# Kernel tuning notes

Hardware: AMD Instinct MI355X
Metric: run time of the kernel (lower is better)

## Reference

```python
import jax, jax.numpy as jnp
import numpy as np

Q_MAX = 127.0  # int8 symmetric quant range


def setup_inputs() -> dict:
    key = jax.random.key(0)
    kx, kw, ks = jax.random.split(key, 3)
    M, K, N = 16384, 4096, 4096
    x = jax.random.normal(kx, (M, K), dtype=jnp.float32)
    # int8 weight values in [-127, 127]
    weight = jax.random.randint(kw, (N, K), -127, 128, dtype=jnp.int32).astype(jnp.int8)
    # per-output-row dequant scale, small positive values as a real quantizer would produce
    weight_scale = jax.random.uniform(ks, (N, 1), dtype=jnp.float32, minval=1e-3, maxval=1e-2)
    return {"x": x, "weight": weight, "weight_scale": weight_scale}


def reference(x, weight, weight_scale):
    # --- per-token dynamic activation quantization (get_hip_quant(per_Token)) ---
    amax = jnp.max(jnp.abs(x), axis=-1, keepdims=True)            # [M,1]
    x_scale = amax / Q_MAX                                        # [M,1]
    x_q = jnp.clip(jnp.round(x / jnp.maximum(x_scale, 1e-8)), -Q_MAX, Q_MAX)  # int8 values, kept fp32
    # --- gemm_a8w8: int8xint8 GEMM with fused dequant (row scale_a * col scale_b) ---
    acc = jnp.einsum('mk,nk->mn', x_q, weight.astype(jnp.float32),
                     preferred_element_type=jnp.float32)          # [M,N] int accumulation in fp32
    y = acc * x_scale * weight_scale.T                            # fused dequant scales
    return y  # fp32 stand-in for otype=bf16 output
```

## Files before the change

kernel.cpp:

```cpp
#include <hip/hip_runtime.h>
#include <stdint.h>

#define M_DIM 16384
#define N_DIM 4096
#define K_DIM 4096

#define BM 256
#define BN 128
#define BK 128

typedef int i32x4 __attribute__((ext_vector_type(4)));

__device__ __forceinline__ void async16(const uint8_t* g, uint8_t* l) {
    __builtin_amdgcn_global_load_lds(
        (const __attribute__((address_space(1))) void*)g,
        (__attribute__((address_space(3))) void*)l,
        16, 0, 0);
}

__global__ __launch_bounds__(256) void pack_w_kernel(const int* __restrict__ w32,
                                                     uint32_t* __restrict__ w8,
                                                     int n4) {
    int i = blockIdx.x * 256 + threadIdx.x;
    if (i < n4) {
        const int4 v = reinterpret_cast<const int4*>(w32)[i];
        uint32_t p = (uint32_t)(v.x & 255) | ((uint32_t)(v.y & 255) << 8) |
                     ((uint32_t)(v.z & 255) << 16) | ((uint32_t)(v.w & 255) << 24);
        w8[i] = p;
    }
}

__global__ __launch_bounds__(256) void quant_kernel(const float* __restrict__ x,
                                                    uint32_t* __restrict__ xq,
                                                    float* __restrict__ xscale) {
    const int m = blockIdx.x;
    const int t = threadIdx.x;
    const float4* row = reinterpret_cast<const float4*>(x + (size_t)m * K_DIM);
    float4 v[4];
    float amax = 0.0f;
#pragma unroll
    for (int i = 0; i < 4; ++i) {
        v[i] = row[t + i * 256];
        amax = fmaxf(amax, fmaxf(fmaxf(fabsf(v[i].x), fabsf(v[i].y)),
                                 fmaxf(fabsf(v[i].z), fabsf(v[i].w))));
    }
#pragma unroll
    for (int off = 32; off > 0; off >>= 1) amax = fmaxf(amax, __shfl_xor(amax, off));
    __shared__ float smax[4];
    if ((t & 63) == 0) smax[t >> 6] = amax;
    __syncthreads();
    amax = fmaxf(fmaxf(smax[0], smax[1]), fmaxf(smax[2], smax[3]));
    const float scale = amax / 127.0f;
    const float s = fmaxf(scale, 1e-8f);
    if (t == 0) xscale[m] = scale;
    uint32_t* orow = xq + (size_t)m * (K_DIM / 4);
#pragma unroll
    for (int i = 0; i < 4; ++i) {
        int q0 = __float2int_rn(v[i].x / s);
        int q1 = __float2int_rn(v[i].y / s);
        int q2 = __float2int_rn(v[i].z / s);
        int q3 = __float2int_rn(v[i].w / s);
        q0 = max(-127, min(127, q0));
        q1 = max(-127, min(127, q1));
        q2 = max(-127, min(127, q2));
        q3 = max(-127, min(127, q3));
        uint32_t p = (uint32_t)(q0 & 255) | ((uint32_t)(q1 & 255) << 8) |
                     ((uint32_t)(q2 & 255) << 16) | ((uint32_t)(q3 & 255) << 24);
        orow[t + i * 256] = p;
    }
}

__global__ __launch_bounds__(256, 2) void gemm_kernel(
    const uint8_t* __restrict__ Aq, const float* __restrict__ ascale,
    const uint8_t* __restrict__ Bq, const float* __restrict__ wscale,
    float* __restrict__ out) {
    __shared__ uint8_t lds[BM * BK + BN * BK];
    uint8_t* ldsA = lds;
    uint8_t* ldsB = lds + BM * BK;

    const int tid = threadIdx.x;
    const int lane = tid & 63;
    const int w = tid >> 6;
    const int wr = w >> 1;
    const int wc = w & 1;
    const int lr = lane & 15;
    const int lg = lane >> 4;

    const size_t row0 = (size_t)blockIdx.y * BM;
    const size_t col0 = (size_t)blockIdx.x * BN;
    const uint8_t* aBase = Aq + row0 * K_DIM;
    const uint8_t* bBase = Bq + col0 * K_DIM;

    i32x4 acc[8][4];
#pragma unroll
    for (int i = 0; i < 8; ++i)
#pragma unroll
        for (int j = 0; j < 4; ++j) acc[i][j] = (i32x4){0, 0, 0, 0};

    for (int k0 = 0; k0 < K_DIM; k0 += BK) {
#pragma unroll
        for (int it = 0; it < 8; ++it) {
            const int idx = it * 256 + tid;
            const int m = idx >> 3, p = idx & 7;
            const uint8_t* src = aBase + (size_t)m * K_DIM + k0 + ((p ^ (m & 7)) << 4);
            async16(src, ldsA + (it * 256 + w * 64) * 16);
        }
#pragma unroll
        for (int it = 0; it < 4; ++it) {
            const int idx = it * 256 + tid;
            const int n = idx >> 3, p = idx & 7;
            const uint8_t* src = bBase + (size_t)n * K_DIM + k0 + ((p ^ (n & 7)) << 4);
            async16(src, ldsB + (it * 256 + w * 64) * 16);
        }
        __syncthreads();

#pragma unroll
        for (int kk = 0; kk < 2; ++kk) {
            i32x4 af[8], bf[4];
#pragma unroll
            for (int mf = 0; mf < 8; ++mf) {
                const int r = wr * 128 + mf * 16 + lr;
                const int u = kk * 4 + lg;
                af[mf] = *reinterpret_cast<const i32x4*>(
                    ldsA + r * BK + ((u ^ (r & 7)) << 4));
            }
#pragma unroll
            for (int nf = 0; nf < 4; ++nf) {
                const int r = wc * 64 + nf * 16 + lr;
                const int u = kk * 4 + lg;
                bf[nf] = *reinterpret_cast<const i32x4*>(
                    ldsB + r * BK + ((u ^ (r & 7)) << 4));
            }
#pragma unroll
            for (int mf = 0; mf < 8; ++mf)
#pragma unroll
                for (int nf = 0; nf < 4; ++nf)
                    acc[mf][nf] = __builtin_amdgcn_mfma_i32_16x16x64_i8(
                        af[mf], bf[nf], acc[mf][nf], 0, 0, 0);
        }
        __syncthreads();
    }

    const float* asp = ascale + row0 + wr * 128;
    const float* wsp = wscale + col0 + wc * 64;
    float wsv[4];
#pragma unroll
    for (int nf = 0; nf < 4; ++nf) wsv[nf] = wsp[nf * 16 + lr];
    float* outBase = out + (row0 + wr * 128) * (size_t)N_DIM + col0 + wc * 64;
#pragma unroll
    for (int mf = 0; mf < 8; ++mf) {
#pragma unroll
        for (int j = 0; j < 4; ++j) {
            const int r = mf * 16 + lg * 4 + j;
            const float av = asp[r];
            float* orow = outBase + (size_t)r * N_DIM;
#pragma unroll
            for (int nf = 0; nf < 4; ++nf) {
                orow[nf * 16 + lr] = (float)acc[mf][nf][j] * av * wsv[nf];
            }
        }
    }
}

extern "C" void kernel_launch(void* const* d_in, const int* in_sizes, int n_in,
                              void* d_out, int out_size, void* d_ws, size_t ws_size,
                              hipStream_t stream) {
    const float* x = (const float*)d_in[0];
    const int* w32 = (const int*)d_in[1];
    const float* wscale = (const float*)d_in[2];
    float* out = (float*)d_out;

    uint8_t* ws = (uint8_t*)d_ws;
    uint32_t* xq = (uint32_t*)ws;
    float* xscale = (float*)(ws + (size_t)M_DIM * K_DIM);
    uint8_t* wq = ws + (size_t)M_DIM * K_DIM + (size_t)M_DIM * 4;

    pack_w_kernel<<<dim3((N_DIM * K_DIM / 4 + 255) / 256), 256, 0, stream>>>(
        w32, (uint32_t*)wq, N_DIM * K_DIM / 4);
    quant_kernel<<<dim3(M_DIM), 256, 0, stream>>>(x, xq, xscale);
    gemm_kernel<<<dim3(N_DIM / BN, M_DIM / BM), 256, 0, stream>>>(
        (const uint8_t*)xq, xscale, wq, wscale, out);
}
```

Baseline: 369.2 us.

## Double-buffer LDS with interleaved async staging in a 256x256 GEMM tile, 8 waves

Enlarges the GEMM tile to 256x256 with 512 threads (8 waves) and double-buffers the A/B tiles in LDS. Async global-to-LDS loads for upcoming K-steps are interleaved with MFMA quadrants, gated by explicit vmcnt waits and barriers, and s_setprio raises wave priority around the MFMA blocks. A 1D grid with swizzled block mapping is meant to improve L2 reuse. LDS use rises to 128KB per block, which lowers occupancy, and the hand-tuned waitcnt ordering risks races if the counts are off.

```diff
diff --git a/kernel.cpp b/kernel.cpp
--- a/kernel.cpp
+++ b/kernel.cpp
@@ -6,8 +6,9 @@
 #define K_DIM 4096
 
 #define BM 256
-#define BN 128
+#define BN 256
 #define BK 128
+#define NT (K_DIM / BK)
 
 typedef int i32x4 __attribute__((ext_vector_type(4)));
 
@@ -70,26 +71,32 @@
     }
 }
 
-__global__ __launch_bounds__(256, 2) void gemm_kernel(
+__global__ __launch_bounds__(512, 2) void gemm_kernel(
     const uint8_t* __restrict__ Aq, const float* __restrict__ ascale,
     const uint8_t* __restrict__ Bq, const float* __restrict__ wscale,
     float* __restrict__ out) {
-    __shared__ uint8_t lds[BM * BK + BN * BK];
-    uint8_t* ldsA = lds;
-    uint8_t* ldsB = lds + BM * BK;
+    __shared__ uint8_t lds[2 * BM * BK + 2 * BN * BK];
+    uint8_t* ldsA0 = lds;
+    uint8_t* ldsA1 = lds + BM * BK;
+    uint8_t* ldsB0 = lds + 2 * BM * BK;
+    uint8_t* ldsB1 = lds + 2 * BM * BK + BN * BK;
 
     const int tid = threadIdx.x;
     const int lane = tid & 63;
     const int w = tid >> 6;
-    const int wr = w >> 1;
-    const int wc = w & 1;
+    const int wr = w >> 2;
+    const int wc = w & 3;
     const int lr = lane & 15;
     const int lg = lane >> 4;
-
-    const size_t row0 = (size_t)blockIdx.y * BM;
-    const size_t col0 = (size_t)blockIdx.x * BN;
-    const uint8_t* aBase = Aq + row0 * K_DIM;
-    const uint8_t* bBase = Bq + col0 * K_DIM;
+    const int aa = lane >> 3;
+    const int pp = lane & 7;
+
+    const int bid = blockIdx.x;
+    const int swz = (bid & 7) * (1024 / 8) + (bid >> 3);
+    const size_t row0 = (size_t)(swz >> 4) * BM;
+    const size_t col0 = (size_t)(swz & 15) * BN;
+    const uint8_t* Ab = Aq + row0 * K_DIM;
+    const uint8_t* Bb = Bq + col0 * K_DIM;
 
     i32x4 acc[8][4];
 #pragma unroll
@@ -97,48 +104,132 @@
 #pragma unroll
         for (int j = 0; j < 4; ++j) acc[i][j] = (i32x4){0, 0, 0, 0};
 
-    for (int k0 = 0; k0 < K_DIM; k0 += BK) {
-#pragma unroll
-        for (int it = 0; it < 8; ++it) {
-            const int idx = it * 256 + tid;
-            const int m = idx >> 3, p = idx & 7;
-            const uint8_t* src = aBase + (size_t)m * K_DIM + k0 + ((p ^ (m & 7)) << 4);
-            async16(src, ldsA + (it * 256 + w * 64) * 16);
-        }
-#pragma unroll
-        for (int it = 0; it < 4; ++it) {
-            const int idx = it * 256 + tid;
-            const int n = idx >> 3, p = idx & 7;
-            const uint8_t* src = bBase + (size_t)n * K_DIM + k0 + ((p ^ (n & 7)) << 4);
-            async16(src, ldsB + (it * 256 + w * 64) * 16);
-        }
-        __syncthreads();
-
-#pragma unroll
-        for (int kk = 0; kk < 2; ++kk) {
-            i32x4 af[8], bf[4];
-#pragma unroll
-            for (int mf = 0; mf < 8; ++mf) {
-                const int r = wr * 128 + mf * 16 + lr;
-                const int u = kk * 4 + lg;
-                af[mf] = *reinterpret_cast<const i32x4*>(
-                    ldsA + r * BK + ((u ^ (r & 7)) << 4));
-            }
-#pragma unroll
-            for (int nf = 0; nf < 4; ++nf) {
-                const int r = wc * 64 + nf * 16 + lr;
-                const int u = kk * 4 + lg;
-                bf[nf] = *reinterpret_cast<const i32x4*>(
-                    ldsB + r * BK + ((u ^ (r & 7)) << 4));
-            }
-#pragma unroll
-            for (int mf = 0; mf < 8; ++mf)
-#pragma unroll
-                for (int nf = 0; nf < 4; ++nf)
-                    acc[mf][nf] = __builtin_amdgcn_mfma_i32_16x16x64_i8(
-                        af[mf], bf[nf], acc[mf][nf], 0, 0, 0);
-        }
-        __syncthreads();
+#define STAGE_A(DST, KT, MH)                                                     \
+    do {                                                                         \
+        _Pragma("unroll") for (int it_ = 0; it_ < 2; ++it_) {                    \
+            const int m_ = (MH) * 64 + w * 8 + aa + it_ * 128;                   \
+            async16(Ab + (size_t)m_ * K_DIM + (KT) * BK + ((pp ^ aa) << 4),      \
+                    (DST) + ((MH) * 64 + w * 8 + it_ * 128) * BK);               \
+        }                                                                        \
+    } while (0)
+
+#define STAGE_B(DST, KT, NH)                                                     \
+    do {                                                                         \
+        _Pragma("unroll") for (int it_ = 0; it_ < 2; ++it_) {                    \
+            const int rwh_ = it_ * 64 + w * 8 + aa;                              \
+            const int n_ = (NH) * 32 + (rwh_ & 31) + ((rwh_ >> 5) << 6);         \
+            const int rw0_ = it_ * 64 + w * 8;                                   \
+            const int nb_ = (NH) * 32 + (rw0_ & 31) + ((rw0_ >> 5) << 6);        \
+            async16(Bb + (size_t)n_ * K_DIM + (KT) * BK + ((pp ^ aa) << 4),      \
+                    (DST) + nb_ * BK);                                           \
+        }                                                                        \
+    } while (0)
+
+#define READ_A(BUF, MH)                                                          \
+    do {                                                                         \
+        _Pragma("unroll") for (int mf_ = 0; mf_ < 4; ++mf_)                      \
+        _Pragma("unroll") for (int kk_ = 0; kk_ < 2; ++kk_) {                    \
+            const int r_ = wr * 128 + (MH) * 64 + mf_ * 16 + lr;                 \
+            const int u_ = kk_ * 4 + lg;                                         \
+            af[mf_][kk_] = *reinterpret_cast<const i32x4*>(                      \
+                (BUF) + r_ * BK + ((u_ ^ (r_ & 7)) << 4));                       \
+        }                                                                        \
+    } while (0)
+
+#define READ_B(BUF, NH, DSTF)                                                    \
+    do {                                                                         \
+        _Pragma("unroll") for (int nf_ = 0; nf_ < 2; ++nf_)                      \
+        _Pragma("unroll") for (int kk_ = 0; kk_ < 2; ++kk_) {                    \
+            const int r_ = wc * 64 + (NH) * 32 + nf_ * 16 + lr;                  \
+            const int u_ = kk_ * 4 + lg;                                         \
+            DSTF[nf_][kk_] = *reinterpret_cast<const i32x4*>(                    \
+                (BUF) + r_ * BK + ((u_ ^ (r_ & 7)) << 4));                       \
+        }                                                                        \
+    } while (0)
+
+#define MFMA_QUAD(MH, NH, BF)                                                    \
+    do {                                                                         \
+        __builtin_amdgcn_s_setprio(1);                                           \
+        _Pragma("unroll") for (int mf_ = 0; mf_ < 4; ++mf_)                      \
+        _Pragma("unroll") for (int nf_ = 0; nf_ < 2; ++nf_)                      \
+        _Pragma("unroll") for (int kk_ = 0; kk_ < 2; ++kk_)                      \
+            acc[(MH) * 4 + mf_][(NH) * 2 + nf_] =                                \
+                __builtin_amdgcn_mfma_i32_16x16x64_i8(                           \
+                    af[mf_][kk_], BF[nf_][kk_],                                  \
+                    acc[(MH) * 4 + mf_][(NH) * 2 + nf_], 0, 0, 0);               \
+        __builtin_amdgcn_s_setprio(0);                                           \
+    } while (0)
+
+#define BAR __builtin_amdgcn_s_barrier()
+#define VMCNT6 asm volatile("s_waitcnt vmcnt(6)" ::: "memory")
+
+    STAGE_A(ldsA0, 0, 0);
+    STAGE_A(ldsA0, 0, 1);
+    STAGE_B(ldsB0, 0, 0);
+    STAGE_B(ldsB0, 0, 1);
+    STAGE_A(ldsA1, 1, 0);
+    STAGE_B(ldsB1, 1, 0);
+    STAGE_B(ldsB1, 1, 1);
+    VMCNT6;
+    BAR;
+
+    i32x4 af[4][2], bfA[2][2], bfB[2][2];
+
+#pragma unroll 1
+    for (int it2 = 0; it2 < NT / 2; ++it2) {
+        const int t = 2 * it2;
+        const int kt2 = (t + 2 < NT) ? t + 2 : NT - 1;
+        const int kt3 = (t + 3 < NT) ? t + 3 : NT - 1;
+
+        READ_A(ldsA0, 0);
+        READ_B(ldsB0, 0, bfA);
+        STAGE_A(ldsA1, t + 1, 1);
+        BAR;
+        MFMA_QUAD(0, 0, bfA);
+        BAR;
+
+        READ_B(ldsB0, 1, bfB);
+        STAGE_A(ldsA0, kt2, 0);
+        BAR;
+        MFMA_QUAD(0, 1, bfB);
+        BAR;
+
+        READ_A(ldsA0, 1);
+        STAGE_B(ldsB0, kt2, 0);
+        BAR;
+        MFMA_QUAD(1, 1, bfB);
+        BAR;
+
+        STAGE_B(ldsB0, kt2, 1);
+        BAR;
+        MFMA_QUAD(1, 0, bfA);
+        VMCNT6;
+        BAR;
+
+        READ_A(ldsA1, 0);
+        READ_B(ldsB1, 0, bfA);
+        STAGE_A(ldsA0, kt2, 1);
+        BAR;
+        MFMA_QUAD(0, 0, bfA);
+        BAR;
+
+        READ_B(ldsB1, 1, bfB);
+        STAGE_A(ldsA1, kt3, 0);
+        BAR;
+        MFMA_QUAD(0, 1, bfB);
+        BAR;
+
+        READ_A(ldsA1, 1);
+        STAGE_B(ldsB1, kt3, 0);
+        BAR;
+        MFMA_QUAD(1, 1, bfB);
+        BAR;
+
+        STAGE_B(ldsB1, kt3, 1);
+        BAR;
+        MFMA_QUAD(1, 0, bfA);
+        VMCNT6;
+        BAR;
     }
 
     const float* asp = ascale + row0 + wr * 128;
@@ -160,6 +251,13 @@
             }
         }
     }
+#undef STAGE_A
+#undef STAGE_B
+#undef READ_A
+#undef READ_B
+#undef MFMA_QUAD
+#undef BAR
+#undef VMCNT6
 }
 
 extern "C" void kernel_launch(void* const* d_in, const int* in_sizes, int n_in,
@@ -178,6 +276,6 @@
     pack_w_kernel<<<dim3((N_DIM * K_DIM / 4 + 255) / 256), 256, 0, stream>>>(
         w32, (uint32_t*)wq, N_DIM * K_DIM / 4);
     quant_kernel<<<dim3(M_DIM), 256, 0, stream>>>(x, xq, xscale);
-    gemm_kernel<<<dim3(N_DIM / BN, M_DIM / BM), 256, 0, stream>>>(
+    gemm_kernel<<<dim3((M_DIM / BM) * (N_DIM / BN)), 512, 0, stream>>>(
         (const uint8_t*)xq, xscale, wq, wscale, out);
 }
```

Result: faster. 346.5 us (-6.2%).
